# Optimization experiments

Measured on AMD Instinct MI355X. Metric: run time of the kernel, lower is better.

## Reference

```python
import jax, jax.numpy as jnp
import numpy as np

# Hyperparameters (from __init__ defaults)
TIME_RES = 25
BASE_RES = 512
MAX_RES = 32768
N_LEVELS = 8
N_FEATS = 4
LOG2_HASHMAP = 13
HASHMAP_SIZE = 1 << LOG2_HASHMAP  # 8192
PRIME_Y = np.uint32(2654435761)   # instant-ngp 2D hash prime (dim0 prime is 1)

# Per-level grid scales (tcnn convention: scale = 2^(l*log2_pls)*base - 1)
_LOG2_PLS = np.log2(MAX_RES / BASE_RES) / (N_LEVELS - 1)
SCALES = jnp.asarray(np.exp2(np.arange(N_LEVELS) * _LOG2_PLS) * BASE_RES - 1.0,
                     dtype=jnp.float32)  # [L]


def _hash_encode(x, table_t):
    """Instant-NGP 2D multires hash encoding for one time slice.
    x: [N,2] in [0,1); table_t: [L, H, F]. Returns [N, L*F].
    All levels satisfy res^2 > HASHMAP_SIZE, so always the hash path."""
    N = x.shape[0]
    pos = x[:, None, :] * SCALES[None, :, None] + 0.5        # [N,L,2]
    pos_i = jnp.floor(pos)
    frac = pos - pos_i                                        # [N,L,2]
    pos_i = pos_i.astype(jnp.uint32)
    lvl = jnp.arange(N_LEVELS, dtype=jnp.int32)[None, :]      # [1,L]
    acc = jnp.zeros((N, N_LEVELS, N_FEATS), dtype=table_t.dtype)
    mask = jnp.uint32(HASHMAP_SIZE - 1)
    for dx in (0, 1):  # 4 bilinear corners (static unroll)
        for dy in (0, 1):
            ix = pos_i[..., 0] + jnp.uint32(dx)               # [N,L]
            iy = pos_i[..., 1] + jnp.uint32(dy)
            h = jnp.bitwise_xor(ix, iy * PRIME_Y) & mask      # [N,L] hash index
            w = (frac[..., 0] if dx else 1.0 - frac[..., 0]) * \
                (frac[..., 1] if dy else 1.0 - frac[..., 1])  # [N,L]
            f = table_t[lvl, h.astype(jnp.int32)]             # [N,L,F] gather
            acc = acc + w[..., None] * f
    return acc.reshape(N, N_LEVELS * N_FEATS)


def setup_inputs() -> dict:
    key = jax.random.key(0)
    k1, k2 = jax.random.split(key)
    N = 2_000_000
    x = jax.random.uniform(k1, (N, 2), dtype=jnp.float32)
    t = jnp.asarray(0.3, dtype=jnp.float32)  # scalar time in [0,1]
    # tcnn initializes hash tables uniform in [-1e-4, 1e-4]
    table = jax.random.uniform(k2, (TIME_RES, N_LEVELS, HASHMAP_SIZE, N_FEATS),
                               dtype=jnp.float32, minval=-1e-4, maxval=1e-4)
    return {"x": x, "t": t, "table": table}


def reference(x, t, table):
    idx = t * (TIME_RES - 1)
    i1 = jnp.floor(idx).astype(jnp.int32)
    i2 = jnp.ceil(idx).astype(jnp.int32)
    # blend weight; equals (i2-idx, idx-i1) when i1!=i2 and (1,0) when equal,
    # matching the torch branch semantics.
    w2 = idx - i1.astype(idx.dtype)
    w1 = 1.0 - w2
    tab1 = jax.lax.dynamic_index_in_dim(table, i1, axis=0, keepdims=False)
    tab2 = jax.lax.dynamic_index_in_dim(table, i2, axis=0, keepdims=False)
    f1 = _hash_encode(x, tab1)  # [N, 32]
    f2 = _hash_encode(x, tab2)
    return w1 * f1 + w2 * f2
```

## Files before the change

### kernel.cpp

```cpp
#include <hip/hip_runtime.h>
#include <hip/hip_fp16.h>
#include <math.h>

#define NLV 8
#define NF 4
#define HSZ 8192
#define TRES 25
#define PRIME 2654435761u

struct Scales { float s[NLV]; };

__global__ __launch_bounds__(256) void blend_kernel(
    const float* __restrict__ table, const float* __restrict__ tptr,
    __half2* __restrict__ bt)
{
    int i = blockIdx.x * 256 + threadIdx.x;
    float t = *tptr;
    float idx = t * (float)(TRES - 1);
    float fi1 = floorf(idx);
    float fi2 = ceilf(idx);
    float w2 = idx - fi1;
    float w1 = 1.0f - w2;
    size_t off1 = (size_t)(int)fi1 * (size_t)(NLV * HSZ * NF);
    size_t off2 = (size_t)(int)fi2 * (size_t)(NLV * HSZ * NF);
    float4 a = ((const float4*)(table + off1))[i];
    float4 b = ((const float4*)(table + off2))[i];
    float4 r;
    r.x = w1 * a.x + w2 * b.x;
    r.y = w1 * a.y + w2 * b.y;
    r.z = w1 * a.z + w2 * b.z;
    r.w = w1 * a.w + w2 * b.w;
    bt[2 * (size_t)i]     = __floats2half2_rn(r.x, r.y);
    bt[2 * (size_t)i + 1] = __floats2half2_rn(r.z, r.w);
}

__device__ __forceinline__ float2 h2f(unsigned u) {
    return __half22float2(__builtin_bit_cast(__half2, u));
}

__device__ __forceinline__ float4 gather_lvl(const uint2* tbl, float2 p, float scale)
{
    float px = __fadd_rn(__fmul_rn(p.x, scale), 0.5f);
    float py = __fadd_rn(__fmul_rn(p.y, scale), 0.5f);
    float fx0 = floorf(px), fy0 = floorf(py);
    float fx = px - fx0, fy = py - fy0;
    unsigned ix = (unsigned)(int)fx0;
    unsigned iy = (unsigned)(int)fy0;
    unsigned hy0 = iy * PRIME;
    unsigned hy1 = hy0 + PRIME;
    unsigned h00 = (ix         ^ hy0) & (HSZ - 1);
    unsigned h01 = (ix         ^ hy1) & (HSZ - 1);
    unsigned h10 = ((ix + 1u)  ^ hy0) & (HSZ - 1);
    unsigned h11 = ((ix + 1u)  ^ hy1) & (HSZ - 1);
    uint2 v00 = tbl[h00];
    uint2 v01 = tbl[h01];
    uint2 v10 = tbl[h10];
    uint2 v11 = tbl[h11];
    float gx = 1.0f - fx, gy = 1.0f - fy;
    float w00 = gx * gy, w01 = gx * fy, w10 = fx * gy, w11 = fx * fy;
    float2 a00 = h2f(v00.x), b00 = h2f(v00.y);
    float2 a01 = h2f(v01.x), b01 = h2f(v01.y);
    float2 a10 = h2f(v10.x), b10 = h2f(v10.y);
    float2 a11 = h2f(v11.x), b11 = h2f(v11.y);
    float4 r;
    r.x = w00 * a00.x + w01 * a01.x + w10 * a10.x + w11 * a11.x;
    r.y = w00 * a00.y + w01 * a01.y + w10 * a10.y + w11 * a11.y;
    r.z = w00 * b00.x + w01 * b01.x + w10 * b10.x + w11 * b11.x;
    r.w = w00 * b00.y + w01 * b01.y + w10 * b10.y + w11 * b11.y;
    return r;
}

__global__ __launch_bounds__(1024, 4) void encode_kernel(
    const float* __restrict__ x, const float4* __restrict__ bt,
    float* __restrict__ out, int npts, Scales sc)
{
    __shared__ float4 smem[2][4096];
    int tid = threadIdx.x;
    int base = blockIdx.x * 2048 + tid;
    int n0 = base, n1 = base + 1024;
    int c0 = n0 < npts ? n0 : npts - 1;
    int c1 = n1 < npts ? n1 : npts - 1;
    float2 p0 = ((const float2*)x)[c0];
    float2 p1 = ((const float2*)x)[c1];

    float4 acc0[NLV], acc1[NLV];

    {
        const float4* src = bt;
        smem[0][tid]        = src[tid];
        smem[0][tid + 1024] = src[tid + 1024];
        smem[0][tid + 2048] = src[tid + 2048];
        smem[0][tid + 3072] = src[tid + 3072];
    }
    __syncthreads();

    #pragma unroll
    for (int l = 0; l < NLV; ++l) {
        float4 s0, s1, s2, s3;
        if (l < NLV - 1) {
            const float4* src = bt + (size_t)(l + 1) * 4096;
            s0 = src[tid];        s1 = src[tid + 1024];
            s2 = src[tid + 2048]; s3 = src[tid + 3072];
        }

        const uint2* tbl = (const uint2*)smem[l & 1];
        float scale = sc.s[l];
        acc0[l] = gather_lvl(tbl, p0, scale);
        acc1[l] = gather_lvl(tbl, p1, scale);

        if (l < NLV - 1) {
            float4* dst = smem[(l & 1) ^ 1];
            dst[tid] = s0; dst[tid + 1024] = s1;
            dst[tid + 2048] = s2; dst[tid + 3072] = s3;
            __syncthreads();
        }
    }

    if (n0 < npts) {
        float4* o = (float4*)(out + (size_t)n0 * 32);
        #pragma unroll
        for (int l = 0; l < NLV; ++l) o[l] = acc0[l];
    }
    if (n1 < npts) {
        float4* o = (float4*)(out + (size_t)n1 * 32);
        #pragma unroll
        for (int l = 0; l < NLV; ++l) o[l] = acc1[l];
    }
}

extern "C" void kernel_launch(void* const* d_in, const int* in_sizes, int n_in,
                              void* d_out, int out_size, void* d_ws, size_t ws_size,
                              hipStream_t stream) {
    const float* x     = (const float*)d_in[0];
    const float* t     = (const float*)d_in[1];
    const float* table = (const float*)d_in[2];
    float* out = (float*)d_out;
    __half2* bt = (__half2*)d_ws;

    int npts = in_sizes[0] / 2;

    Scales sc;
    const double l2p = log2(32768.0 / 512.0) / 7.0;
    for (int l = 0; l < NLV; ++l)
        sc.s[l] = (float)(exp2((double)l * l2p) * 512.0 - 1.0);

    blend_kernel<<<(NLV * HSZ) / 256, 256, 0, stream>>>(table, t, bt);

    int nblocks = (npts + 2047) / 2048;
    encode_kernel<<<nblocks, 1024, 0, stream>>>(
        x, (const float4*)bt, out, npts, sc);
}
```

Before: 459.6 us.

## Stage hash-table levels into LDS with direct global-to-LDS async loads

Replaces the register-staged double-buffer copy of each level's blended hash table into shared memory with direct global_load_lds transfers, using manual vmcnt waits and raw barriers to pipeline the next level's load with the current level's gathers. This removes the VGPR cost and the explicit LDS store instructions of the staging. It also drops the occupancy hint from the launch bounds. The correctness depends on the vmcnt counting and barrier placement being right, including the x loads issued earlier. 16-byte global_load_lds requires hardware support such as gfx950.

```diff
diff --git a/kernel.cpp b/kernel.cpp
--- a/kernel.cpp
+++ b/kernel.cpp
@@ -70,7 +70,19 @@
     return r;
 }
 
-__global__ __launch_bounds__(1024, 4) void encode_kernel(
+__device__ __forceinline__ void stage_dma(const float4* __restrict__ src,
+                                          float4* dst, int tid)
+{
+    #pragma unroll
+    for (int k = 0; k < 4; ++k) {
+        __builtin_amdgcn_global_load_lds(
+            (const __attribute__((address_space(1))) unsigned int*)(src + tid + k * 1024),
+            (__attribute__((address_space(3))) unsigned int*)(dst + tid + k * 1024),
+            16, 0, 0);
+    }
+}
+
+__global__ __launch_bounds__(1024) void encode_kernel(
     const float* __restrict__ x, const float4* __restrict__ bt,
     float* __restrict__ out, int npts, Scales sc)
 {
@@ -85,23 +97,17 @@
 
     float4 acc0[NLV], acc1[NLV];
 
-    {
-        const float4* src = bt;
-        smem[0][tid]        = src[tid];
-        smem[0][tid + 1024] = src[tid + 1024];
-        smem[0][tid + 2048] = src[tid + 2048];
-        smem[0][tid + 3072] = src[tid + 3072];
-    }
-    __syncthreads();
+    stage_dma(bt, smem[0], tid);
 
     #pragma unroll
     for (int l = 0; l < NLV; ++l) {
-        float4 s0, s1, s2, s3;
-        if (l < NLV - 1) {
-            const float4* src = bt + (size_t)(l + 1) * 4096;
-            s0 = src[tid];        s1 = src[tid + 1024];
-            s2 = src[tid + 2048]; s3 = src[tid + 3072];
-        }
+        if (l < NLV - 1)
+            stage_dma(bt + (size_t)(l + 1) * 4096, smem[(l + 1) & 1], tid);
+
+        if (l < NLV - 1) asm volatile("s_waitcnt vmcnt(4)" ::: "memory");
+        else             asm volatile("s_waitcnt vmcnt(0)" ::: "memory");
+        __builtin_amdgcn_s_barrier();
+        __builtin_amdgcn_sched_barrier(0);
 
         const uint2* tbl = (const uint2*)smem[l & 1];
         float scale = sc.s[l];
@@ -109,10 +115,8 @@
         acc1[l] = gather_lvl(tbl, p1, scale);
 
         if (l < NLV - 1) {
-            float4* dst = smem[(l & 1) ^ 1];
-            dst[tid] = s0; dst[tid + 1024] = s1;
-            dst[tid + 2048] = s2; dst[tid + 3072] = s3;
-            __syncthreads();
+            __builtin_amdgcn_sched_barrier(0);
+            __builtin_amdgcn_s_barrier();
         }
     }
 
```

New measurement: 418.2 us. -9.0%, faster.
